# Performance work log

Measured on AMD Instinct MI355X. Metric: run time of the kernel, lower is better.

## Reference

```python
import jax, jax.numpy as jnp
import numpy as np

B, S, C = 4, 2048, 768
H = 6
D = C // H  # head_dim = 128


def setup_inputs() -> dict:
    key = jax.random.key(0)
    k_x, k_wa, k_ba, k_wp, k_bp = jax.random.split(key, 5)
    scale = 1.0 / np.sqrt(C)
    return {
        "x": jax.random.normal(k_x, (B, S, C), dtype=jnp.float32),
        "w_attn": jax.random.normal(k_wa, (C, 3 * C), dtype=jnp.float32) * scale,
        "b_attn": jax.random.normal(k_ba, (3 * C,), dtype=jnp.float32) * 0.02,
        "w_proj": jax.random.normal(k_wp, (C, C), dtype=jnp.float32) * scale,
        "b_proj": jax.random.normal(k_bp, (C,), dtype=jnp.float32) * 0.02,
    }


def reference(x, w_attn, b_attn, w_proj, b_proj):
    Bb, Ss, Cc = x.shape
    qkv = x @ w_attn + b_attn                      # [B,S,3C]
    q, k, v = jnp.split(qkv, 3, axis=-1)
    # [B,S,C] -> [B,H,S,D]
    q = q.reshape(Bb, Ss, H, D).transpose(0, 2, 1, 3)
    k = k.reshape(Bb, Ss, H, D).transpose(0, 2, 1, 3)
    v = v.reshape(Bb, Ss, H, D).transpose(0, 2, 1, 3)
    scores = jnp.einsum("bhsd,bhtd->bhst", q, k) / jnp.sqrt(jnp.float32(D))
    causal = jnp.tril(jnp.ones((Ss, Ss), dtype=bool))  # [S,S]
    scores = jnp.where(causal[None, None], scores, -jnp.inf)
    attn = jax.nn.softmax(scores, axis=-1)             # [B,H,S,S]
    out = jnp.einsum("bhst,bhtd->bhsd", attn, v)       # [B,H,S,D]
    out = out.transpose(0, 2, 1, 3).reshape(Bb, Ss, Cc)
    return out @ w_proj + b_proj
```

## Files before the change

kernel.cpp:

```cpp
#include <hip/hip_runtime.h>
#include <hip/hip_bf16.h>
#include <stdint.h>

#define SS 2048
#define CC 768
#define C3 2304
#define NITEMS (64 * 24)
#define QSC 0.08838834764831845f

typedef float f32x4 __attribute__((ext_vector_type(4)));
typedef short s16x8 __attribute__((ext_vector_type(8)));

__device__ __forceinline__ unsigned short f2bf(float f) {
  union { float f; unsigned int u; } v; v.f = f;
  unsigned int r = (v.u + 0x7FFFu + ((v.u >> 16) & 1u)) >> 16;
  return (unsigned short)r;
}

__device__ __forceinline__ s16x8 ld8(const unsigned short* p) {
  return *reinterpret_cast<const s16x8*>(p);
}

__device__ __forceinline__ unsigned int cvt_pk_bf16(float lo, float hi) {
  unsigned int r;
  asm("v_cvt_pk_bf16_f32 %0, %1, %2" : "=v"(r) : "v"(lo), "v"(hi));
  return r;
}

__device__ __forceinline__ void gload_lds16(const unsigned short* g, unsigned short* l) {
  __builtin_amdgcn_global_load_lds(
      (const __attribute__((address_space(1))) void*)g,
      (__attribute__((address_space(3))) void*)l, 16, 0, 0);
}

__global__ __launch_bounds__(256) void cast_bf16_kernel(
    const float* __restrict__ src, unsigned short* __restrict__ dst, int n4) {
  int i = blockIdx.x * 256 + threadIdx.x;
  if (i < n4) {
    float4 v = reinterpret_cast<const float4*>(src)[i];
    ushort4 o;
    o.x = f2bf(v.x); o.y = f2bf(v.y); o.z = f2bf(v.z); o.w = f2bf(v.w);
    reinterpret_cast<ushort4*>(dst)[i] = o;
  }
}

__global__ __launch_bounds__(256) void transpose_cast_kernel(
    const float* __restrict__ src, unsigned short* __restrict__ dst, int R, int C,
    int nsc) {
  __shared__ float tile[32][33];
  int c0 = blockIdx.x * 32, r0 = blockIdx.y * 32;
  int tx = threadIdx.x & 31, ty = threadIdx.x >> 5;
  #pragma unroll
  for (int i = 0; i < 32; i += 8)
    tile[ty + i][tx] = src[(size_t)(r0 + ty + i) * C + c0 + tx];
  __syncthreads();
  #pragma unroll
  for (int i = 0; i < 32; i += 8) {
    int oc = c0 + ty + i;
    float v = tile[tx][ty + i];
    if (oc < nsc) v *= QSC;
    dst[(size_t)oc * R + r0 + tx] = f2bf(v);
  }
}

__global__ __launch_bounds__(256) void vtrans_kernel(
    const unsigned short* __restrict__ qkv, unsigned short* __restrict__ vT) {
  __shared__ unsigned short t[64 * 128];
  const int tid = threadIdx.x;
  const int n0 = blockIdx.x * 64;
  const int bh = blockIdx.y;
  const int b = bh / 6, h = bh % 6;
  #pragma unroll
  for (int it = 0; it < 4; ++it) {
    int c = it * 256 + tid;
    int n = c >> 4, slot = c & 15;
    s16x8 v = ld8(qkv + (size_t)(b * SS + n0 + n) * C3 + 2 * CC + h * 128 + slot * 8);
    int ss = slot ^ ((n >> 3) & 7);
    *reinterpret_cast<s16x8*>(&t[n * 128 + ss * 8]) = v;
  }
  __syncthreads();
  #pragma unroll
  for (int it = 0; it < 4; ++it) {
    int c = it * 256 + tid;
    int d = c >> 3, n8 = (c & 7) * 8;
    s16x8 o;
    #pragma unroll
    for (int j = 0; j < 8; ++j) {
      int n = n8 + j;
      int sl = (d >> 3) ^ ((n >> 3) & 7);
      o[j] = (short)t[n * 128 + sl * 8 + (d & 7)];
    }
    *reinterpret_cast<s16x8*>(&vT[((size_t)bh * 128 + d) * SS + n0 + n8]) = o;
  }
}

template <int OUT_BF16>
__global__ __launch_bounds__(256) void gemm_lds_kernel(
    const unsigned short* __restrict__ A, const unsigned short* __restrict__ Bt,
    const float* __restrict__ bias, void* __restrict__ out, int M, int N, int K,
    int nsc) {
  __shared__ unsigned short lA[2][128 * 32];
  __shared__ unsigned short lB[2][128 * 32];
  const int tid = threadIdx.x, lane = tid & 63, w = tid >> 6;
  const int nbx = gridDim.x;
  int bid = blockIdx.y * nbx + blockIdx.x;
  const int cpx = (nbx * gridDim.y) >> 3;
  bid = (bid & 7) * cpx + (bid >> 3);
  const int m0 = (bid / nbx) * 128, n0 = (bid % nbx) * 128;
  const int lm = lane & 15, lg = lane >> 4;
  const int wm = (w >> 1) * 64, wn = (w & 1) * 64;
  const int sr = lane >> 2;
  const int ssl = ((lane & 3) ^ ((sr >> 1) & 3)) * 8;
  int aOff[4], bOff[4];
  #pragma unroll
  for (int i = 0; i < 4; ++i) {
    int ra = wm + i * 16 + lm, rb = wn + i * 16 + lm;
    aOff[i] = ra * 32 + ((lg ^ ((ra >> 1) & 3)) * 8);
    bOff[i] = rb * 32 + ((lg ^ ((rb >> 1) & 3)) * 8);
  }
  f32x4 acc[4][4] = {};
  const int nt = K / 32;
  #define GSTAGE(tt, bb)                                                      \
    {                                                                         \
      const int k0_ = (tt) * 32;                                              \
      _Pragma("unroll")                                                       \
      for (int i_ = 0; i_ < 2; ++i_) {                                        \
        int c_ = w * 2 + i_;                                                  \
        int row_ = c_ * 16 + sr;                                              \
        gload_lds16(A + (size_t)(m0 + row_) * K + k0_ + ssl, &lA[bb][c_ * 512]); \
        gload_lds16(Bt + (size_t)(n0 + row_) * K + k0_ + ssl, &lB[bb][c_ * 512]); \
      }                                                                       \
    }
  GSTAGE(0, 0);
  #pragma unroll 1
  for (int t = 0; t < nt; ++t) {
    if (t + 1 < nt) {
      GSTAGE(t + 1, (t + 1) & 1);
      asm volatile("s_waitcnt vmcnt(4)" ::: "memory");
    } else {
      asm volatile("s_waitcnt vmcnt(0)" ::: "memory");
    }
    __builtin_amdgcn_sched_barrier(0);
    __builtin_amdgcn_s_barrier();
    const int cu = t & 1;
    s16x8 af[4], bf[4];
    #pragma unroll
    for (int i = 0; i < 4; ++i) af[i] = ld8(&lA[cu][aOff[i]]);
    #pragma unroll
    for (int i = 0; i < 4; ++i) bf[i] = ld8(&lB[cu][bOff[i]]);
    __builtin_amdgcn_s_setprio(1);
    #pragma unroll
    for (int mi = 0; mi < 4; ++mi)
      #pragma unroll
      for (int ni = 0; ni < 4; ++ni)
        acc[mi][ni] = __builtin_amdgcn_mfma_f32_16x16x32_bf16(af[mi], bf[ni], acc[mi][ni], 0, 0, 0);
    __builtin_amdgcn_s_setprio(0);
    asm volatile("s_waitcnt lgkmcnt(0)" ::: "memory");
    __builtin_amdgcn_sched_barrier(0);
    __builtin_amdgcn_s_barrier();
  }
  #pragma unroll
  for (int mi = 0; mi < 4; ++mi) {
    #pragma unroll
    for (int ni = 0; ni < 4; ++ni) {
      const int row = m0 + wm + mi * 16 + lg * 4;
      const int col = n0 + wn + ni * 16 + lm;
      float bs = bias[col];
      if (col < nsc) bs *= QSC;
      #pragma unroll
      for (int r = 0; r < 4; ++r) {
        float v = acc[mi][ni][r] + bs;
        if (OUT_BF16)
          ((unsigned short*)out)[(size_t)(row + r) * N + col] = f2bf(v);
        else
          ((float*)out)[(size_t)(row + r) * N + col] = v;
      }
    }
  }
  #undef GSTAGE
}

__global__ __launch_bounds__(128) void attn_kernel(
    const unsigned short* __restrict__ qkv,
    const unsigned short* __restrict__ vT,
    unsigned short* __restrict__ aout,
    int* __restrict__ ctr) {
  const int tid = threadIdx.x, lane = tid & 63, w = tid >> 6;
  const int lm = lane & 15, lg = lane >> 4;
  __shared__ unsigned short kbuf[64 * 128];
  __shared__ unsigned short vbuf[128 * 64];
  __shared__ unsigned int pb[2][16 * 36];
  __shared__ int s_item;
  unsigned int* pr = &pb[w][lm * 36];
  const int klg4 = lane >> 4, ks16 = lane & 15;
  const int vlg8 = lane >> 3, vs8 = lane & 7;
  for (;;) {
    __syncthreads();
    if (tid == 0) s_item = atomicAdd(ctr, 1);
    __syncthreads();
    const int item = s_item;
    if (item >= NITEMS) return;
    const int qt = 63 - (item / 24);
    const int bh = item % 24;
    const int b = bh / 6, h = bh % 6;
    const int wq0 = qt * 32 + w * 16;
    const unsigned short* base = qkv + (size_t)b * SS * C3;
    const unsigned short* kg = base + CC + h * 128;
    const unsigned short* vg = vT + (size_t)bh * 128 * SS;
    s16x8 qf[4];
    {
      const unsigned short* qp = base + (size_t)(wq0 + lm) * C3 + h * 128 + lg * 8;
      #pragma unroll
      for (int ks = 0; ks < 4; ++ks) qf[ks] = ld8(qp + ks * 32);
    }
    #define AK(tt)                                                            \
      {                                                                       \
        const int n1_ = (tt) * 64;                                            \
        _Pragma("unroll")                                                     \
        for (int i_ = 0; i_ < 8; ++i_) {                                      \
          int c_ = w * 8 + i_;                                                \
          int r_ = c_ * 4 + klg4;                                             \
          gload_lds16(kg + (size_t)(n1_ + r_) * C3 + ((ks16 ^ (r_ & 7)) * 8), \
                      &kbuf[c_ * 512]);                                       \
        }                                                                     \
      }
    #define AV(tt)                                                            \
      {                                                                       \
        const int n1_ = (tt) * 64;                                            \
        _Pragma("unroll")                                                     \
        for (int i_ = 0; i_ < 8; ++i_) {                                      \
          int c_ = w * 8 + i_;                                                \
          int d_ = c_ * 8 + vlg8;                                             \
          gload_lds16(vg + (size_t)d_ * SS + n1_ + ((vs8 ^ (d_ & 7)) * 8),    \
                      &vbuf[c_ * 512]);                                       \
        }                                                                     \
      }
    f32x4 oacc[8] = {};
    float m_run = -1e30f, l_run = 0.0f;
    const int nt = (qt >> 1) + 1;
    AK(0);
    AV(0);
    #pragma unroll 1
    for (int t = 0; t < nt; ++t) {
      asm volatile("s_waitcnt vmcnt(8)" ::: "memory");
      __builtin_amdgcn_sched_barrier(0);
      __builtin_amdgcn_s_barrier();
      const int n0 = t * 64;
      f32x4 sacc[4] = {};
      __builtin_amdgcn_s_setprio(1);
      #pragma unroll
      for (int nsub = 0; nsub < 4; ++nsub) {
        const int kr = (nsub * 16 + lm) * 128;
        #pragma unroll
        for (int ks = 0; ks < 4; ++ks) {
          s16x8 kf = ld8(&kbuf[kr + (((ks * 4 + lg) ^ (lm & 7)) * 8)]);
          sacc[nsub] = __builtin_amdgcn_mfma_f32_16x16x32_bf16(kf, qf[ks], sacc[nsub], 0, 0, 0);
        }
      }
      __builtin_amdgcn_s_setprio(0);
      asm volatile("s_waitcnt lgkmcnt(0)" ::: "memory");
      __builtin_amdgcn_sched_barrier(0);
      __builtin_amdgcn_s_barrier();
      if (t + 1 < nt) AK(t + 1);
      const int qg = wq0 + lm;
      const bool full = (n0 + 63 <= wq0);
      float xs[4][4];
      float tmax = -1e30f;
      #pragma unroll
      for (int nsub = 0; nsub < 4; ++nsub) {
        #pragma unroll
        for (int r = 0; r < 4; ++r) {
          int n = n0 + nsub * 16 + lg * 4 + r;
          float x = sacc[nsub][r];
          if (!full && n > qg) x = -1e30f;
          xs[nsub][r] = x;
          tmax = fmaxf(tmax, x);
        }
      }
      tmax = fmaxf(tmax, __shfl_xor(tmax, 16));
      tmax = fmaxf(tmax, __shfl_xor(tmax, 32));
      const bool noresc = __all(tmax - m_run <= 8.0f);
      const float m_new = noresc ? m_run : fmaxf(m_run, tmax);
      float psum = 0.0f;
      unsigned int pk_[4][2];
      #pragma unroll
      for (int nsub = 0; nsub < 4; ++nsub) {
        float p0 = __expf(xs[nsub][0] - m_new);
        float p1 = __expf(xs[nsub][1] - m_new);
        float p2 = __expf(xs[nsub][2] - m_new);
        float p3 = __expf(xs[nsub][3] - m_new);
        psum += (p0 + p1) + (p2 + p3);
        pk_[nsub][0] = cvt_pk_bf16(p0, p1);
        pk_[nsub][1] = cvt_pk_bf16(p2, p3);
      }
      psum += __shfl_xor(psum, 16);
      psum += __shfl_xor(psum, 32);
      if (!noresc) {
        const float resc = __expf(m_run - m_new);
        l_run *= resc;
        m_run = m_new;
        float rs[4];
        #pragma unroll
        for (int r = 0; r < 4; ++r) rs[r] = __shfl(resc, lg * 4 + r);
        #pragma unroll
        for (int dsub = 0; dsub < 8; ++dsub)
          #pragma unroll
          for (int r = 0; r < 4; ++r) oacc[dsub][r] *= rs[r];
      }
      l_run += psum;
      #pragma unroll
      for (int nsub = 0; nsub < 4; ++nsub) {
        uint2 pk2; pk2.x = pk_[nsub][0]; pk2.y = pk_[nsub][1];
        *reinterpret_cast<uint2*>(&pr[nsub * 8 + lg * 2]) = pk2;
      }
      if (t + 1 < nt) {
        asm volatile("s_waitcnt vmcnt(8)" ::: "memory");
      } else {
        asm volatile("s_waitcnt vmcnt(0)" ::: "memory");
      }
      __builtin_amdgcn_sched_barrier(0);
      __builtin_amdgcn_s_barrier();
      __builtin_amdgcn_s_setprio(1);
      #pragma unroll
      for (int nch = 0; nch < 2; ++nch) {
        s16x8 pf = *reinterpret_cast<const s16x8*>(&pr[nch * 16 + lg * 4]);
        #pragma unroll
        for (int dsub = 0; dsub < 8; ++dsub) {
          const int vr = (dsub * 16 + lm) * 64;
          s16x8 vf = ld8(&vbuf[vr + (((nch * 4 + lg) ^ (lm & 7)) * 8)]);
          oacc[dsub] = __builtin_amdgcn_mfma_f32_16x16x32_bf16(pf, vf, oacc[dsub], 0, 0, 0);
        }
      }
      __builtin_amdgcn_s_setprio(0);
      asm volatile("s_waitcnt lgkmcnt(0)" ::: "memory");
      __builtin_amdgcn_sched_barrier(0);
      __builtin_amdgcn_s_barrier();
      if (t + 1 < nt) AV(t + 1);
    }
    #undef AK
    #undef AV
    float linv[4];
    #pragma unroll
    for (int r = 0; r < 4; ++r) linv[r] = 1.0f / __shfl(l_run, lg * 4 + r);
    #pragma unroll
    for (int dsub = 0; dsub < 8; ++dsub) {
      const int col = h * 128 + dsub * 16 + lm;
      #pragma unroll
      for (int r = 0; r < 4; ++r)
        aout[(size_t)(b * SS + wq0 + lg * 4 + r) * CC + col] =
            f2bf(oacc[dsub][r] * linv[r]);
    }
  }
}

extern "C" void kernel_launch(void* const* d_in, const int* in_sizes, int n_in,
                              void* d_out, int out_size, void* d_ws, size_t ws_size,
                              hipStream_t stream) {
  const float* x      = (const float*)d_in[0];
  const float* w_attn = (const float*)d_in[1];
  const float* b_attn = (const float*)d_in[2];
  const float* w_proj = (const float*)d_in[3];
  const float* b_proj = (const float*)d_in[4];
  float* out = (float*)d_out;

  const size_t M = 4 * (size_t)SS;
  unsigned short* ws = (unsigned short*)d_ws;
  unsigned short* xb   = ws;
  unsigned short* waT  = xb + M * CC;
  unsigned short* wpT  = waT + (size_t)C3 * CC;
  unsigned short* qkv  = wpT + (size_t)CC * CC;
  unsigned short* aout = qkv + M * C3;
  unsigned short* vT   = xb;
  int* ctr = (int*)(aout + M * CC);

  int n4 = (int)(M * CC / 4);
  cast_bf16_kernel<<<(n4 + 255) / 256, 256, 0, stream>>>(x, xb, n4);
  transpose_cast_kernel<<<dim3(C3 / 32, CC / 32), 256, 0, stream>>>(w_attn, waT, CC, C3, CC);
  transpose_cast_kernel<<<dim3(CC / 32, CC / 32), 256, 0, stream>>>(w_proj, wpT, CC, CC, 0);

  gemm_lds_kernel<1><<<dim3(C3 / 128, M / 128), 256, 0, stream>>>(
      xb, waT, b_attn, (void*)qkv, (int)M, C3, CC, CC);

  vtrans_kernel<<<dim3(SS / 64, 24), 256, 0, stream>>>(qkv, vT);

  hipMemsetAsync(ctr, 0, sizeof(int), stream);
  attn_kernel<<<1024, 128, 0, stream>>>(qkv, vT, aout, ctr);

  gemm_lds_kernel<0><<<dim3(CC / 128, M / 128), 256, 0, stream>>>(
      aout, wpT, b_proj, (void*)out, (int)M, CC, CC, 0);
}
```

Before: 173.4 us.

## Use 64-row query tiles with 4 waves per attention block and reorder items

```diff
diff --git a/kernel.cpp b/kernel.cpp
--- a/kernel.cpp
+++ b/kernel.cpp
@@ -5,7 +5,7 @@
 #define SS 2048
 #define CC 768
 #define C3 2304
-#define NITEMS (64 * 24)
+#define NITEMS 768
 #define QSC 0.08838834764831845f
 
 typedef float f32x4 __attribute__((ext_vector_type(4)));
@@ -180,7 +180,7 @@
   #undef GSTAGE
 }
 
-__global__ __launch_bounds__(128) void attn_kernel(
+__global__ __launch_bounds__(256) void attn_kernel(
     const unsigned short* __restrict__ qkv,
     const unsigned short* __restrict__ vT,
     unsigned short* __restrict__ aout,
@@ -189,7 +189,7 @@
   const int lm = lane & 15, lg = lane >> 4;
   __shared__ unsigned short kbuf[64 * 128];
   __shared__ unsigned short vbuf[128 * 64];
-  __shared__ unsigned int pb[2][16 * 36];
+  __shared__ unsigned int pb[4][16 * 36];
   __shared__ int s_item;
   unsigned int* pr = &pb[w][lm * 36];
   const int klg4 = lane >> 4, ks16 = lane & 15;
@@ -200,10 +200,12 @@
     __syncthreads();
     const int item = s_item;
     if (item >= NITEMS) return;
-    const int qt = 63 - (item / 24);
-    const int bh = item % 24;
+    const int j = item & 255, g = item >> 8;
+    const int r = (g == 0) ? j : ((g == 1) ? 767 - j : 256 + j);
+    const int qt = 31 - (r / 24);
+    const int bh = r % 24;
     const int b = bh / 6, h = bh % 6;
-    const int wq0 = qt * 32 + w * 16;
+    const int wq0 = qt * 64 + w * 16;
     const unsigned short* base = qkv + (size_t)b * SS * C3;
     const unsigned short* kg = base + CC + h * 128;
     const unsigned short* vg = vT + (size_t)bh * 128 * SS;
@@ -217,8 +219,8 @@
       {                                                                       \
         const int n1_ = (tt) * 64;                                            \
         _Pragma("unroll")                                                     \
-        for (int i_ = 0; i_ < 8; ++i_) {                                      \
-          int c_ = w * 8 + i_;                                                \
+        for (int i_ = 0; i_ < 4; ++i_) {                                      \
+          int c_ = w * 4 + i_;                                                \
           int r_ = c_ * 4 + klg4;                                             \
           gload_lds16(kg + (size_t)(n1_ + r_) * C3 + ((ks16 ^ (r_ & 7)) * 8), \
                       &kbuf[c_ * 512]);                                       \
@@ -228,8 +230,8 @@
       {                                                                       \
         const int n1_ = (tt) * 64;                                            \
         _Pragma("unroll")                                                     \
-        for (int i_ = 0; i_ < 8; ++i_) {                                      \
-          int c_ = w * 8 + i_;                                                \
+        for (int i_ = 0; i_ < 4; ++i_) {                                      \
+          int c_ = w * 4 + i_;                                                \
           int d_ = c_ * 8 + vlg8;                                             \
           gload_lds16(vg + (size_t)d_ * SS + n1_ + ((vs8 ^ (d_ & 7)) * 8),    \
                       &vbuf[c_ * 512]);                                       \
@@ -237,101 +239,112 @@
       }
     f32x4 oacc[8] = {};
     float m_run = -1e30f, l_run = 0.0f;
-    const int nt = (qt >> 1) + 1;
+    const int nt = qt + 1;
     AK(0);
     AV(0);
     #pragma unroll 1
     for (int t = 0; t < nt; ++t) {
-      asm volatile("s_waitcnt vmcnt(8)" ::: "memory");
+      const int n0 = t * 64;
+      const bool active = (n0 <= wq0 + 15);
+      if (t + 1 < nt) {
+        asm volatile("s_waitcnt vmcnt(4)" ::: "memory");
+      } else {
+        asm volatile("s_waitcnt vmcnt(4)" ::: "memory");
+      }
       __builtin_amdgcn_sched_barrier(0);
       __builtin_amdgcn_s_barrier();
-      const int n0 = t * 64;
       f32x4 sacc[4] = {};
-      __builtin_amdgcn_s_setprio(1);
-      #pragma unroll
-      for (int nsub = 0; nsub < 4; ++nsub) {
-        const int kr = (nsub * 16 + lm) * 128;
+      if (active) {
+        __builtin_amdgcn_s_setprio(1);
         #pragma unroll
-        for (int ks = 0; ks < 4; ++ks) {
-          s16x8 kf = ld8(&kbuf[kr + (((ks * 4 + lg) ^ (lm & 7)) * 8)]);
-          sacc[nsub] = __builtin_amdgcn_mfma_f32_16x16x32_bf16(kf, qf[ks], sacc[nsub], 0, 0, 0);
-        }
-      }
-      __builtin_amdgcn_s_setprio(0);
+        for (int nsub = 0; nsub < 4; ++nsub) {
+          const int kr = (nsub * 16 + lm) * 128;
+          #pragma unroll
+          for (int ks = 0; ks < 4; ++ks) {
+            s16x8 kf = ld8(&kbuf[kr + (((ks * 4 + lg) ^ (lm & 7)) * 8)]);
+            sacc[nsub] = __builtin_amdgcn_mfma_f32_16x16x32_bf16(kf, qf[ks], sacc[nsub], 0, 0, 0);
+          }
+        }
+        __builtin_amdgcn_s_setprio(0);
+      }
       asm volatile("s_waitcnt lgkmcnt(0)" ::: "memory");
       __builtin_amdgcn_sched_barrier(0);
       __builtin_amdgcn_s_barrier();
       if (t + 1 < nt) AK(t + 1);
-      const int qg = wq0 + lm;
-      const bool full = (n0 + 63 <= wq0);
-      float xs[4][4];
-      float tmax = -1e30f;
-      #pragma unroll
-      for (int nsub = 0; nsub < 4; ++nsub) {
+      if (active) {
+        const int qg = wq0 + lm;
+        const bool full = (n0 + 63 <= wq0);
+        float xs[4][4];
+        float tmax = -1e30f;
         #pragma unroll
-        for (int r = 0; r < 4; ++r) {
-          int n = n0 + nsub * 16 + lg * 4 + r;
-          float x = sacc[nsub][r];
-          if (!full && n > qg) x = -1e30f;
-          xs[nsub][r] = x;
-          tmax = fmaxf(tmax, x);
-        }
-      }
-      tmax = fmaxf(tmax, __shfl_xor(tmax, 16));
-      tmax = fmaxf(tmax, __shfl_xor(tmax, 32));
-      const bool noresc = __all(tmax - m_run <= 8.0f);
-      const float m_new = noresc ? m_run : fmaxf(m_run, tmax);
-      float psum = 0.0f;
-      unsigned int pk_[4][2];
-      #pragma unroll
-      for (int nsub = 0; nsub < 4; ++nsub) {
-        float p0 = __expf(xs[nsub][0] - m_new);
-        float p1 = __expf(xs[nsub][1] - m_new);
-        float p2 = __expf(xs[nsub][2] - m_new);
-        float p3 = __expf(xs[nsub][3] - m_new);
-        psum += (p0 + p1) + (p2 + p3);
-        pk_[nsub][0] = cvt_pk_bf16(p0, p1);
-        pk_[nsub][1] = cvt_pk_bf16(p2, p3);
-      }
-      psum += __shfl_xor(psum, 16);
-      psum += __shfl_xor(psum, 32);
-      if (!noresc) {
-        const float resc = __expf(m_run - m_new);
-        l_run *= resc;
-        m_run = m_new;
-        float rs[4];
+        for (int nsub = 0; nsub < 4; ++nsub) {
+          #pragma unroll
+          for (int rr = 0; rr < 4; ++rr) {
+            int n = n0 + nsub * 16 + lg * 4 + rr;
+            float x = sacc[nsub][rr];
+            if (!full && n > qg) x = -1e30f;
+            xs[nsub][rr] = x;
+            tmax = fmaxf(tmax, x);
+          }
+        }
+        tmax = fmaxf(tmax, __shfl_xor(tmax, 16));
+        tmax = fmaxf(tmax, __shfl_xor(tmax, 32));
+        const bool noresc = __all(tmax - m_run <= 8.0f);
+        const float m_new = noresc ? m_run : fmaxf(m_run, tmax);
+        float psum = 0.0f;
+        unsigned int pk_[4][2];
         #pragma unroll
-        for (int r = 0; r < 4; ++r) rs[r] = __shfl(resc, lg * 4 + r);
+        for (int nsub = 0; nsub < 4; ++nsub) {
+          float p0 = __expf(xs[nsub][0] - m_new);
+          float p1 = __expf(xs[nsub][1] - m_new);
+          float p2 = __expf(xs[nsub][2] - m_new);
+          float p3 = __expf(xs[nsub][3] - m_new);
+          psum += (p0 + p1) + (p2 + p3);
+          pk_[nsub][0] = cvt_pk_bf16(p0, p1);
+          pk_[nsub][1] = cvt_pk_bf16(p2, p3);
+        }
+        psum += __shfl_xor(psum, 16);
+        psum += __shfl_xor(psum, 32);
+        if (!noresc) {
+          const float resc = __expf(m_run - m_new);
+          l_run *= resc;
+          m_run = m_new;
+          float rs[4];
+          #pragma unroll
+          for (int rr = 0; rr < 4; ++rr) rs[rr] = __shfl(resc, lg * 4 + rr);
+          #pragma unroll
+          for (int dsub = 0; dsub < 8; ++dsub)
+            #pragma unroll
+            for (int rr = 0; rr < 4; ++rr) oacc[dsub][rr] *= rs[rr];
+        }
+        l_run += psum;
         #pragma unroll
-        for (int dsub = 0; dsub < 8; ++dsub)
-          #pragma unroll
-          for (int r = 0; r < 4; ++r) oacc[dsub][r] *= rs[r];
-      }
-      l_run += psum;
-      #pragma unroll
-      for (int nsub = 0; nsub < 4; ++nsub) {
-        uint2 pk2; pk2.x = pk_[nsub][0]; pk2.y = pk_[nsub][1];
-        *reinterpret_cast<uint2*>(&pr[nsub * 8 + lg * 2]) = pk2;
+        for (int nsub = 0; nsub < 4; ++nsub) {
+          uint2 pk2; pk2.x = pk_[nsub][0]; pk2.y = pk_[nsub][1];
+          *reinterpret_cast<uint2*>(&pr[nsub * 8 + lg * 2]) = pk2;
+        }
       }
       if (t + 1 < nt) {
-        asm volatile("s_waitcnt vmcnt(8)" ::: "memory");
+        asm volatile("s_waitcnt vmcnt(4)" ::: "memory");
       } else {
         asm volatile("s_waitcnt vmcnt(0)" ::: "memory");
       }
       __builtin_amdgcn_sched_barrier(0);
       __builtin_amdgcn_s_barrier();
-      __builtin_amdgcn_s_setprio(1);
-      #pragma unroll
-      for (int nch = 0; nch < 2; ++nch) {
-        s16x8 pf = *reinterpret_cast<const s16x8*>(&pr[nch * 16 + lg * 4]);
+      if (active) {
+        __builtin_amdgcn_s_setprio(1);
         #pragma unroll
-        for (int dsub = 0; dsub < 8; ++dsub) {
-          const int vr = (dsub * 16 + lm) * 64;
-          s16x8 vf = ld8(&vbuf[vr + (((nch * 4 + lg) ^ (lm & 7)) * 8)]);
-          oacc[dsub] = __builtin_amdgcn_mfma_f32_16x16x32_bf16(pf, vf, oacc[dsub], 0, 0, 0);
-        }
-      }
-      __builtin_amdgcn_s_setprio(0);
+        for (int nch = 0; nch < 2; ++nch) {
+          s16x8 pf = *reinterpret_cast<const s16x8*>(&pr[nch * 16 + lg * 4]);
+          #pragma unroll
+          for (int dsub = 0; dsub < 8; ++dsub) {
+            const int vr = (dsub * 16 + lm) * 64;
+            s16x8 vf = ld8(&vbuf[vr + (((nch * 4 + lg) ^ (lm & 7)) * 8)]);
+            oacc[dsub] = __builtin_amdgcn_mfma_f32_16x16x32_bf16(pf, vf, oacc[dsub], 0, 0, 0);
+          }
+        }
+        __builtin_amdgcn_s_setprio(0);
+      }
       asm volatile("s_waitcnt lgkmcnt(0)" ::: "memory");
       __builtin_amdgcn_sched_barrier(0);
       __builtin_amdgcn_s_barrier();
@@ -341,14 +354,14 @@
     #undef AV
     float linv[4];
     #pragma unroll
-    for (int r = 0; r < 4; ++r) linv[r] = 1.0f / __shfl(l_run, lg * 4 + r);
+    for (int rr = 0; rr < 4; ++rr) linv[rr] = 1.0f / __shfl(l_run, lg * 4 + rr);
     #pragma unroll
     for (int dsub = 0; dsub < 8; ++dsub) {
       const int col = h * 128 + dsub * 16 + lm;
       #pragma unroll
-      for (int r = 0; r < 4; ++r)
-        aout[(size_t)(b * SS + wq0 + lg * 4 + r) * CC + col] =
-            f2bf(oacc[dsub][r] * linv[r]);
+      for (int rr = 0; rr < 4; ++rr)
+        aout[(size_t)(b * SS + wq0 + lg * 4 + rr) * CC + col] =
+            f2bf(oacc[dsub][rr] * linv[rr]);
     }
   }
 }
@@ -384,7 +397,7 @@
   vtrans_kernel<<<dim3(SS / 64, 24), 256, 0, stream>>>(qkv, vT);
 
   hipMemsetAsync(ctr, 0, sizeof(int), stream);
-  attn_kernel<<<1024, 128, 0, stream>>>(qkv, vT, aout, ctr);
+  attn_kernel<<<768, 256, 0, stream>>>(qkv, vT, aout, ctr);
 
   gemm_lds_kernel<0><<<dim3(CC / 128, M / 128), 256, 0, stream>>>(
       aout, wpT, b_proj, (void*)out, (int)M, CC, CC, 0);
```

After: 169.9 us. 1.02x faster.
